# Performance work log

Measured on AMD Instinct MI355X. Metric: run time of the kernel, lower is better.

The kernel has to match this reference:

```python
import jax, jax.numpy as jnp
import numpy as np

BETA = 6.0

@jax.custom_vjp
def mysign(x):
    e = jnp.exp(BETA * x)
    return ((e - 1.0) / (e + 1.0) + 1.0) / 2.0

def _mysign_fwd(x):
    return mysign(x), x

def _mysign_bwd(x, g):
    e = jnp.exp(BETA * x)
    # faithful to the custom torch backward (extra beta factor vs true gradient)
    return (BETA * (BETA * e) / jnp.square(e + 1.0) * g,)

mysign.defvjp(_mysign_fwd, _mysign_bwd)

N = 4096
E = 262144
EC = 65536
T = 512

def setup_inputs() -> dict:
    key = jax.random.key(0)
    k1, k2, k3, k4, k5 = jax.random.split(key, 5)
    edges = jax.random.randint(k1, (E, 2), 0, N, dtype=jnp.int32)
    weights = jax.random.normal(k2, (E,), dtype=jnp.float32)
    stat = jnp.ones((E,), dtype=jnp.float32)
    edges_c = jax.random.randint(k3, (EC, 2), 0, N, dtype=jnp.int32)
    grdt = jax.random.uniform(k4, (EC,), dtype=jnp.float32)
    targets = jax.random.randint(k5, (T,), 0, N, dtype=jnp.int32)
    return {"edges": edges, "weights": weights, "stat": stat,
            "edges_c": edges_c, "grdt": grdt, "targets": targets, "n": N}

def reference(edges, weights, stat, edges_c, grdt, targets, n):
    # Densify sparse COO tensors (duplicate indices sum, matching torch coalesce)
    W = jnp.zeros((n, n), weights.dtype).at[edges[:, 0], edges[:, 1]].add(weights)
    A = jnp.zeros((n, n), stat.dtype).at[edges[:, 0], edges[:, 1]].add(stat)
    B = jnp.zeros((n, n), grdt.dtype).at[edges_c[:, 0], edges_c[:, 1]].add(grdt)
    V = B * (A - 1.0) + A * W                      # [n, n]

    # Soft degrees: mysign(0) = 0.5, so zero entries each contribute 0.5
    S = mysign(jnp.abs(V))                         # [n, n]
    N_in = S.sum(axis=0)                           # [n]
    N_out = S.sum(axis=1)                          # [n]

    fair0 = jnp.ones((n,), V.dtype)
    good0 = jnp.ones((n,), V.dtype)

    # Goodness update: g[node] = sum_src Fair[src] * V[src, node]
    # (nonzero filter is a no-op here since zero V entries contribute 0)
    g = fair0 @ V                                  # [n]
    good = jnp.where(N_in != 0.0, jnp.clip(g / N_in, -1.0, 1.0), good0)

    # Fairness update: only over actual nonzero out-edges (mask matters here)
    mask = V != 0.0
    contrib = jnp.where(mask, 1.0 - jnp.abs(V - good[None, :]) / 2.0, 0.0)
    f = contrib.sum(axis=1)                        # [n]
    fair = jnp.where(N_out != 0.0, jnp.clip(f / N_out, 0.0, 1.0), fair0)

    gt = good[targets]
    gsum = jnp.sum(jnp.where(jnp.isnan(gt), 0.0, gt))
    # pack objective + updated Fair/Good state into one flat output
    return jnp.concatenate([gsum[None], fair, good])
```

## Files before the change

### kernel.cpp

```cpp
#include <hip/hip_runtime.h>
#include <math.h>

#define NN 4096
#define NPART 8
#define NCHK 128
#define GR 16
#define NGRP 256
#define SCAP 32
#define HS 4096
#define NW 16

__device__ __forceinline__ float smh(float v) {
    float e = expf(6.0f * fabsf(v));
    return 0.5f * (e - 1.0f) / (e + 1.0f);
}

__global__ __launch_bounds__(512) void split_k(
    const long* __restrict__ edges, const float* __restrict__ weights,
    const float* __restrict__ stat, const long* __restrict__ edges_c,
    const float* __restrict__ grdt, float4* __restrict__ subseg,
    int* __restrict__ scnt, int E, int EC) {
    __shared__ float4 stash[64][SCAP];
    __shared__ int cnt[64];
    const int tid = threadIdx.x;
    if (tid < 64) cnt[tid] = 0;
    __syncthreads();
    const int p = blockIdx.x & (NPART - 1);
    const int chunk = blockIdx.x >> 3;
    const int total = E + EC;
    const int csz = (total + NCHK - 1) / NCHK;
    const int lo = chunk * csz;
    const int hi = min(lo + csz, total);
    for (int i = lo + tid; i < hi; i += 512) {
        long e; int isC;
        if (i < E) { e = edges[i]; isC = 0; }
        else { e = edges_c[i - E]; isC = 1; }
        int r = (int)e;
        int c = (int)(e >> 32);
        bool rowHit = (r >> 9) == p;
        bool colHit = (c >> 9) == p;
        if (!rowHit && !colHit) continue;
        float4 rec;
        rec.x = __int_as_float((c << 13) | (r << 1) | isC);
        if (isC) { rec.y = grdt[i - E]; rec.z = 0.f; }
        else { rec.y = stat[i]; rec.z = weights[i]; }
        rec.w = 0.f;
        if (rowHit) {
            int s = (r >> 4) & 31;
            int pos = atomicAdd(&cnt[s], 1);
            if (pos < SCAP) stash[s][pos] = rec;
        }
        if (colHit) {
            int s = 32 + ((c >> 4) & 31);
            int pos = atomicAdd(&cnt[s], 1);
            if (pos < SCAP) stash[s][pos] = rec;
        }
    }
    __syncthreads();
    for (int idx = tid; idx < 64 * SCAP; idx += 512) {
        int s = idx >> 5, i = idx & (SCAP - 1);
        if (i < cnt[s]) {
            int side = s >> 5;
            int grp = p * 32 + (s & 31);
            subseg[(((size_t)side * NGRP + grp) * NCHK + chunk) * SCAP + i]
                = stash[s][i];
        }
    }
    if (tid < 64) {
        int side = tid >> 5;
        int grp = p * 32 + (tid & 31);
        scnt[(side * NGRP + grp) * NCHK + chunk] = min(cnt[tid], SCAP);
    }
}

__global__ __launch_bounds__(1024) void colgood_k(
    const float4* __restrict__ subseg, const int* __restrict__ scnt,
    float* __restrict__ good_buf, float* __restrict__ good_out) {
    __shared__ int hkey[HS];
    __shared__ float hA[HS], hW[HS], hB[HS];
    __shared__ int s_cnt[NCHK];
    __shared__ float a1[GR][NW + 1], a2[GR][NW + 1];
    const int tid = threadIdx.x;
    const int wv = tid >> 6;
    const int g = (blockIdx.x & 7) * 32 + (blockIdx.x >> 3);
    const int cb = g * GR;
    for (int i = tid; i < HS; i += 1024) {
        hkey[i] = -1; hA[i] = 0.f; hW[i] = 0.f; hB[i] = 0.f;
    }
    if (tid < NCHK) s_cnt[tid] = scnt[(NGRP + g) * NCHK + tid];
    if (tid < GR * (NW + 1)) {
        ((float*)a1)[tid] = 0.f;
        ((float*)a2)[tid] = 0.f;
    }
    __syncthreads();
    {
        const int chunk = tid & (NCHK - 1);
        const int sub = tid >> 7;
        const int n = s_cnt[chunk];
        const float4* sp = subseg
            + (((size_t)NGRP + g) * NCHK + chunk) * SCAP;
        for (int i = sub; i < n; i += 8) {
            float4 rec = sp[i];
            int ct = __float_as_int(rec.x);
            int c = ct >> 13;
            int r = (ct >> 1) & 4095;
            int key = ((c - cb) << 12) | r;
            int slot = (int)(((unsigned)key * 2654435761u) >> 20) & (HS - 1);
            while (true) {
                int prev = atomicCAS(&hkey[slot], -1, key);
                if (prev == -1 || prev == key) break;
                slot = (slot + 1) & (HS - 1);
            }
            if (ct & 1) {
                atomicAdd(&hB[slot], rec.y);
            } else {
                atomicAdd(&hA[slot], rec.y);
                atomicAdd(&hW[slot], rec.z);
            }
        }
    }
    __syncthreads();
#pragma unroll
    for (int k = 0; k < HS / 1024; ++k) {
        int s = k * 1024 + tid;
        int key = hkey[s];
        if (key != -1) {
            float a = hA[s], w = hW[s], b = hB[s];
            float v = b * (a - 1.0f) + a * w;
            if (v != 0.0f) {
                int d = key >> 12;
                atomicAdd(&a1[d][wv], smh(v));
                atomicAdd(&a2[d][wv], v);
            }
        }
    }
    __syncthreads();
    if (tid < GR) {
        float nin = 0.f, gsum = 0.f;
        for (int w = 0; w < NW; ++w) { nin += a1[tid][w]; gsum += a2[tid][w]; }
        float Nin = 2048.0f + nin;
        float gd = 1.0f;
        if (Nin != 0.0f) {
            float x = gsum / Nin;
            gd = x < -1.0f ? -1.0f : (x > 1.0f ? 1.0f : x);
        }
        good_buf[cb + tid] = gd;
        good_out[cb + tid] = gd;
    }
}

__global__ __launch_bounds__(1024) void rowfair_k(
    const float4* __restrict__ subseg, const int* __restrict__ scnt,
    const float* __restrict__ good_buf, const int* __restrict__ targets,
    int T, float* __restrict__ out) {
    if (blockIdx.x < NGRP) {
        __shared__ int hkey[HS];
        __shared__ float hA[HS], hW[HS], hB[HS];
        __shared__ int s_cnt[NCHK];
        __shared__ float a1[GR][NW + 1], a2[GR][NW + 1];
        const int tid = threadIdx.x;
        const int wv = tid >> 6;
        const int g = (blockIdx.x & 7) * 32 + (blockIdx.x >> 3);
        const int rb = g * GR;
        for (int i = tid; i < HS; i += 1024) {
            hkey[i] = -1; hA[i] = 0.f; hW[i] = 0.f; hB[i] = 0.f;
        }
        if (tid < NCHK) s_cnt[tid] = scnt[g * NCHK + tid];
        if (tid < GR * (NW + 1)) {
            ((float*)a1)[tid] = 0.f;
            ((float*)a2)[tid] = 0.f;
        }
        __syncthreads();
        {
            const int chunk = tid & (NCHK - 1);
            const int sub = tid >> 7;
            const int n = s_cnt[chunk];
            const float4* sp = subseg + ((size_t)g * NCHK + chunk) * SCAP;
            for (int i = sub; i < n; i += 8) {
                float4 rec = sp[i];
                int ct = __float_as_int(rec.x);
                int c = ct >> 13;
                int r = (ct >> 1) & 4095;
                int key = ((r - rb) << 12) | c;
                int slot = (int)(((unsigned)key * 2654435761u) >> 20) & (HS - 1);
                while (true) {
                    int prev = atomicCAS(&hkey[slot], -1, key);
                    if (prev == -1 || prev == key) break;
                    slot = (slot + 1) & (HS - 1);
                }
                if (ct & 1) {
                    atomicAdd(&hB[slot], rec.y);
                } else {
                    atomicAdd(&hA[slot], rec.y);
                    atomicAdd(&hW[slot], rec.z);
                }
            }
        }
        __syncthreads();
#pragma unroll
        for (int k = 0; k < HS / 1024; ++k) {
            int s = k * 1024 + tid;
            int key = hkey[s];
            if (key != -1) {
                float a = hA[s], w = hW[s], b = hB[s];
                float v = b * (a - 1.0f) + a * w;
                if (v != 0.0f) {
                    int d = key >> 12;
                    atomicAdd(&a1[d][wv], smh(v));
                    atomicAdd(&a2[d][wv],
                              1.0f - 0.5f * fabsf(v - good_buf[key & 4095]));
                }
            }
        }
        __syncthreads();
        if (tid < GR) {
            float nout = 0.f, f = 0.f;
            for (int w = 0; w < NW; ++w) { nout += a1[tid][w]; f += a2[tid][w]; }
            float Nout = 2048.0f + nout;
            float fair = 1.0f;
            if (Nout != 0.0f) {
                float x = f / Nout;
                fair = x < 0.0f ? 0.0f : (x > 1.0f ? 1.0f : x);
            }
            out[1 + rb + tid] = fair;
        }
    } else {
        float s = 0.f;
        for (int i = threadIdx.x; i < T; i += 1024) {
            float gt = good_buf[targets[i]];
            s += (gt == gt) ? gt : 0.0f;
        }
        for (int off = 32; off > 0; off >>= 1) s += __shfl_down(s, off, 64);
        __shared__ float lds[NW];
        int lane = threadIdx.x & 63, w = threadIdx.x >> 6;
        if (lane == 0) lds[w] = s;
        __syncthreads();
        if (threadIdx.x == 0) {
            float tot = 0.f;
            for (int i = 0; i < NW; ++i) tot += lds[i];
            out[0] = tot;
        }
    }
}

extern "C" void kernel_launch(void* const* d_in, const int* in_sizes, int n_in,
                              void* d_out, int out_size, void* d_ws, size_t ws_size,
                              hipStream_t stream) {
    const long*  edges   = (const long*)d_in[0];
    const float* weights = (const float*)d_in[1];
    const float* stat    = (const float*)d_in[2];
    const long*  edges_c = (const long*)d_in[3];
    const float* grdt    = (const float*)d_in[4];
    const int*   targets = (const int*)d_in[5];
    const int E  = in_sizes[1];
    const int EC = in_sizes[4];
    const int T  = in_sizes[5];
    float* out = (float*)d_out;

    int*    scnt     = (int*)d_ws;
    float*  good_buf = (float*)(scnt + 2 * NGRP * NCHK);
    float4* subseg   = (float4*)(good_buf + NN);

    split_k<<<NPART * NCHK, 512, 0, stream>>>(
        edges, weights, stat, edges_c, grdt, subseg, scnt, E, EC);

    colgood_k<<<NGRP, 1024, 0, stream>>>(subseg, scnt, good_buf,
                                         out + 1 + NN);

    rowfair_k<<<NGRP + 1, 1024, 0, stream>>>(subseg, scnt, good_buf,
                                             targets, T, out);
}
```

Measured before the change: 36.39 us.

## Drop row-side bucketing; compute fairness partials from column groups and reduce

Edges are now bucketed only by column group, which halves the split traffic. The column kernel computes good for its 16 columns and then scatters per-row fairness and soft-degree partial sums into a full 4096-row shared array, which each block writes to global memory. A new reduction kernel sums the 256 partial vectors per row and also computes the target sum. This avoids rebuilding a second hash table over the same edges, but it adds writing and reading 2×256×4096 floats of partials and uses more shared memory per block. The hash table shrinks to 2048 slots, which raises the collision risk.

```diff
diff --git a/kernel.cpp b/kernel.cpp
--- a/kernel.cpp
+++ b/kernel.cpp
@@ -7,7 +7,7 @@
 #define GR 16
 #define NGRP 256
 #define SCAP 32
-#define HS 4096
+#define HS 2048
 #define NW 16
 
 __device__ __forceinline__ float smh(float v) {
@@ -20,10 +20,10 @@
     const float* __restrict__ stat, const long* __restrict__ edges_c,
     const float* __restrict__ grdt, float4* __restrict__ subseg,
     int* __restrict__ scnt, int E, int EC) {
-    __shared__ float4 stash[64][SCAP];
-    __shared__ int cnt[64];
+    __shared__ float4 stash[32][SCAP];
+    __shared__ int cnt[32];
     const int tid = threadIdx.x;
-    if (tid < 64) cnt[tid] = 0;
+    if (tid < 32) cnt[tid] = 0;
     __syncthreads();
     const int p = blockIdx.x & (NPART - 1);
     const int chunk = blockIdx.x >> 3;
@@ -37,49 +37,40 @@
         else { e = edges_c[i - E]; isC = 1; }
         int r = (int)e;
         int c = (int)(e >> 32);
-        bool rowHit = (r >> 9) == p;
-        bool colHit = (c >> 9) == p;
-        if (!rowHit && !colHit) continue;
+        if ((c >> 9) != p) continue;
         float4 rec;
         rec.x = __int_as_float((c << 13) | (r << 1) | isC);
         if (isC) { rec.y = grdt[i - E]; rec.z = 0.f; }
         else { rec.y = stat[i]; rec.z = weights[i]; }
         rec.w = 0.f;
-        if (rowHit) {
-            int s = (r >> 4) & 31;
-            int pos = atomicAdd(&cnt[s], 1);
-            if (pos < SCAP) stash[s][pos] = rec;
-        }
-        if (colHit) {
-            int s = 32 + ((c >> 4) & 31);
-            int pos = atomicAdd(&cnt[s], 1);
-            if (pos < SCAP) stash[s][pos] = rec;
-        }
-    }
-    __syncthreads();
-    for (int idx = tid; idx < 64 * SCAP; idx += 512) {
+        int s = (c >> 4) & 31;
+        int pos = atomicAdd(&cnt[s], 1);
+        if (pos < SCAP) stash[s][pos] = rec;
+    }
+    __syncthreads();
+    for (int idx = tid; idx < 32 * SCAP; idx += 512) {
         int s = idx >> 5, i = idx & (SCAP - 1);
         if (i < cnt[s]) {
-            int side = s >> 5;
-            int grp = p * 32 + (s & 31);
-            subseg[(((size_t)side * NGRP + grp) * NCHK + chunk) * SCAP + i]
-                = stash[s][i];
-        }
-    }
-    if (tid < 64) {
-        int side = tid >> 5;
-        int grp = p * 32 + (tid & 31);
-        scnt[(side * NGRP + grp) * NCHK + chunk] = min(cnt[tid], SCAP);
+            int grp = p * 32 + s;
+            subseg[((size_t)grp * NCHK + chunk) * SCAP + i] = stash[s][i];
+        }
+    }
+    if (tid < 32) {
+        int grp = p * 32 + tid;
+        scnt[grp * NCHK + chunk] = min(cnt[tid], SCAP);
     }
 }
 
 __global__ __launch_bounds__(1024) void colgood_k(
     const float4* __restrict__ subseg, const int* __restrict__ scnt,
-    float* __restrict__ good_buf, float* __restrict__ good_out) {
+    float* __restrict__ good_buf, float* __restrict__ good_out,
+    float* __restrict__ fpart, float* __restrict__ npart) {
     __shared__ int hkey[HS];
     __shared__ float hA[HS], hW[HS], hB[HS];
+    __shared__ float s_f[NN], s_n[NN];
     __shared__ int s_cnt[NCHK];
     __shared__ float a1[GR][NW + 1], a2[GR][NW + 1];
+    __shared__ float good_l[GR];
     const int tid = threadIdx.x;
     const int wv = tid >> 6;
     const int g = (blockIdx.x & 7) * 32 + (blockIdx.x >> 3);
@@ -87,7 +78,8 @@
     for (int i = tid; i < HS; i += 1024) {
         hkey[i] = -1; hA[i] = 0.f; hW[i] = 0.f; hB[i] = 0.f;
     }
-    if (tid < NCHK) s_cnt[tid] = scnt[(NGRP + g) * NCHK + tid];
+    for (int i = tid; i < NN; i += 1024) { s_f[i] = 0.f; s_n[i] = 0.f; }
+    if (tid < NCHK) s_cnt[tid] = scnt[g * NCHK + tid];
     if (tid < GR * (NW + 1)) {
         ((float*)a1)[tid] = 0.f;
         ((float*)a2)[tid] = 0.f;
@@ -97,15 +89,14 @@
         const int chunk = tid & (NCHK - 1);
         const int sub = tid >> 7;
         const int n = s_cnt[chunk];
-        const float4* sp = subseg
-            + (((size_t)NGRP + g) * NCHK + chunk) * SCAP;
+        const float4* sp = subseg + ((size_t)g * NCHK + chunk) * SCAP;
         for (int i = sub; i < n; i += 8) {
             float4 rec = sp[i];
             int ct = __float_as_int(rec.x);
             int c = ct >> 13;
             int r = (ct >> 1) & 4095;
             int key = ((c - cb) << 12) | r;
-            int slot = (int)(((unsigned)key * 2654435761u) >> 20) & (HS - 1);
+            int slot = (int)(((unsigned)key * 2654435761u) >> 21) & (HS - 1);
             while (true) {
                 int prev = atomicCAS(&hkey[slot], -1, key);
                 if (prev == -1 || prev == key) break;
@@ -127,9 +118,11 @@
         if (key != -1) {
             float a = hA[s], w = hW[s], b = hB[s];
             float v = b * (a - 1.0f) + a * w;
+            float sv = smh(v);
+            hA[s] = v; hW[s] = sv;
             if (v != 0.0f) {
                 int d = key >> 12;
-                atomicAdd(&a1[d][wv], smh(v));
+                atomicAdd(&a1[d][wv], sv);
                 atomicAdd(&a2[d][wv], v);
             }
         }
@@ -137,109 +130,78 @@
     __syncthreads();
     if (tid < GR) {
         float nin = 0.f, gsum = 0.f;
-        for (int w = 0; w < NW; ++w) { nin += a1[tid][w]; gsum += a2[tid][w]; }
+        for (int w2 = 0; w2 < NW; ++w2) { nin += a1[tid][w2]; gsum += a2[tid][w2]; }
         float Nin = 2048.0f + nin;
         float gd = 1.0f;
         if (Nin != 0.0f) {
             float x = gsum / Nin;
             gd = x < -1.0f ? -1.0f : (x > 1.0f ? 1.0f : x);
         }
+        good_l[tid] = gd;
         good_buf[cb + tid] = gd;
         good_out[cb + tid] = gd;
     }
-}
-
-__global__ __launch_bounds__(1024) void rowfair_k(
-    const float4* __restrict__ subseg, const int* __restrict__ scnt,
+    __syncthreads();
+#pragma unroll
+    for (int k = 0; k < HS / 1024; ++k) {
+        int s = k * 1024 + tid;
+        int key = hkey[s];
+        if (key != -1) {
+            float v = hA[s];
+            if (v != 0.0f) {
+                int r = key & 4095;
+                atomicAdd(&s_n[r], hW[s]);
+                atomicAdd(&s_f[r],
+                          1.0f - 0.5f * fabsf(v - good_l[key >> 12]));
+            }
+        }
+    }
+    __syncthreads();
+    float* fp = fpart + (size_t)blockIdx.x * NN;
+    float* np = npart + (size_t)blockIdx.x * NN;
+    for (int i = tid; i < NN; i += 1024) { fp[i] = s_f[i]; np[i] = s_n[i]; }
+}
+
+__global__ __launch_bounds__(256) void reduce_k(
+    const float* __restrict__ fpart, const float* __restrict__ npart,
     const float* __restrict__ good_buf, const int* __restrict__ targets,
     int T, float* __restrict__ out) {
-    if (blockIdx.x < NGRP) {
-        __shared__ int hkey[HS];
-        __shared__ float hA[HS], hW[HS], hB[HS];
-        __shared__ int s_cnt[NCHK];
-        __shared__ float a1[GR][NW + 1], a2[GR][NW + 1];
+    if (blockIdx.x < NN / GR) {
+        __shared__ float sf[GR][17], sn2[GR][17];
         const int tid = threadIdx.x;
-        const int wv = tid >> 6;
-        const int g = (blockIdx.x & 7) * 32 + (blockIdx.x >> 3);
-        const int rb = g * GR;
-        for (int i = tid; i < HS; i += 1024) {
-            hkey[i] = -1; hA[i] = 0.f; hW[i] = 0.f; hB[i] = 0.f;
-        }
-        if (tid < NCHK) s_cnt[tid] = scnt[g * NCHK + tid];
-        if (tid < GR * (NW + 1)) {
-            ((float*)a1)[tid] = 0.f;
-            ((float*)a2)[tid] = 0.f;
-        }
-        __syncthreads();
-        {
-            const int chunk = tid & (NCHK - 1);
-            const int sub = tid >> 7;
-            const int n = s_cnt[chunk];
-            const float4* sp = subseg + ((size_t)g * NCHK + chunk) * SCAP;
-            for (int i = sub; i < n; i += 8) {
-                float4 rec = sp[i];
-                int ct = __float_as_int(rec.x);
-                int c = ct >> 13;
-                int r = (ct >> 1) & 4095;
-                int key = ((r - rb) << 12) | c;
-                int slot = (int)(((unsigned)key * 2654435761u) >> 20) & (HS - 1);
-                while (true) {
-                    int prev = atomicCAS(&hkey[slot], -1, key);
-                    if (prev == -1 || prev == key) break;
-                    slot = (slot + 1) & (HS - 1);
-                }
-                if (ct & 1) {
-                    atomicAdd(&hB[slot], rec.y);
-                } else {
-                    atomicAdd(&hA[slot], rec.y);
-                    atomicAdd(&hW[slot], rec.z);
-                }
-            }
-        }
-        __syncthreads();
-#pragma unroll
-        for (int k = 0; k < HS / 1024; ++k) {
-            int s = k * 1024 + tid;
-            int key = hkey[s];
-            if (key != -1) {
-                float a = hA[s], w = hW[s], b = hB[s];
-                float v = b * (a - 1.0f) + a * w;
-                if (v != 0.0f) {
-                    int d = key >> 12;
-                    atomicAdd(&a1[d][wv], smh(v));
-                    atomicAdd(&a2[d][wv],
-                              1.0f - 0.5f * fabsf(v - good_buf[key & 4095]));
-                }
-            }
-        }
+        const int rl = tid & 15, sub = tid >> 4;
+        const int r = blockIdx.x * GR + rl;
+        float f = 0.f, n = 0.f;
+        for (int j = 0; j < 16; ++j) {
+            int b = sub * 16 + j;
+            f += fpart[(size_t)b * NN + r];
+            n += npart[(size_t)b * NN + r];
+        }
+        sf[rl][sub] = f; sn2[rl][sub] = n;
         __syncthreads();
         if (tid < GR) {
-            float nout = 0.f, f = 0.f;
-            for (int w = 0; w < NW; ++w) { nout += a1[tid][w]; f += a2[tid][w]; }
-            float Nout = 2048.0f + nout;
+            float F = 0.f, Nn = 0.f;
+            for (int s2 = 0; s2 < 16; ++s2) { F += sf[tid][s2]; Nn += sn2[tid][s2]; }
+            float Nout = 2048.0f + Nn;
             float fair = 1.0f;
             if (Nout != 0.0f) {
-                float x = f / Nout;
+                float x = F / Nout;
                 fair = x < 0.0f ? 0.0f : (x > 1.0f ? 1.0f : x);
             }
-            out[1 + rb + tid] = fair;
+            out[1 + blockIdx.x * GR + tid] = fair;
         }
     } else {
         float s = 0.f;
-        for (int i = threadIdx.x; i < T; i += 1024) {
+        for (int i = threadIdx.x; i < T; i += 256) {
             float gt = good_buf[targets[i]];
             s += (gt == gt) ? gt : 0.0f;
         }
         for (int off = 32; off > 0; off >>= 1) s += __shfl_down(s, off, 64);
-        __shared__ float lds[NW];
+        __shared__ float lds[4];
         int lane = threadIdx.x & 63, w = threadIdx.x >> 6;
         if (lane == 0) lds[w] = s;
         __syncthreads();
-        if (threadIdx.x == 0) {
-            float tot = 0.f;
-            for (int i = 0; i < NW; ++i) tot += lds[i];
-            out[0] = tot;
-        }
+        if (threadIdx.x == 0) out[0] = lds[0] + lds[1] + lds[2] + lds[3];
     }
 }
 
@@ -258,15 +220,17 @@
     float* out = (float*)d_out;
 
     int*    scnt     = (int*)d_ws;
-    float*  good_buf = (float*)(scnt + 2 * NGRP * NCHK);
-    float4* subseg   = (float4*)(good_buf + NN);
+    float*  good_buf = (float*)(scnt + NGRP * NCHK);
+    float*  fpart    = good_buf + NN;
+    float*  npart    = fpart + (size_t)NGRP * NN;
+    float4* subseg   = (float4*)(npart + (size_t)NGRP * NN);
 
     split_k<<<NPART * NCHK, 512, 0, stream>>>(
         edges, weights, stat, edges_c, grdt, subseg, scnt, E, EC);
 
     colgood_k<<<NGRP, 1024, 0, stream>>>(subseg, scnt, good_buf,
-                                         out + 1 + NN);
-
-    rowfair_k<<<NGRP + 1, 1024, 0, stream>>>(subseg, scnt, good_buf,
-                                             targets, T, out);
-}
+                                         out + 1 + NN, fpart, npart);
+
+    reduce_k<<<NN / GR + 1, 256, 0, stream>>>(fpart, npart, good_buf,
+                                              targets, T, out);
+}
```

New measurement: 37.75 us. +3.7%, slower.
